# Kernel tuning notes

Hardware: AMD Instinct MI355X
Metric: run time of the kernel (lower is better)

## Reference

```python
import jax, jax.numpy as jnp
import numpy as np

B, S, HID = 2, 2048, 4096
H, KVH, D = 32, 8, 128
THETA = 10000.0
SCALE = D ** -0.5


def _rope(x, positions):
    # x: [B, S, nH, D], positions: [B, S] int. Neox style: rotate halves.
    half = D // 2
    inv_freq = 1.0 / (THETA ** (jnp.arange(0, half, dtype=jnp.float32) / half))
    ang = positions.astype(jnp.float32)[..., None] * inv_freq  # [B,S,half]
    cos = jnp.cos(ang)[:, :, None, :]  # [B,S,1,half]
    sin = jnp.sin(ang)[:, :, None, :]
    x1, x2 = x[..., :half], x[..., half:]
    return jnp.concatenate([x1 * cos - x2 * sin, x2 * cos + x1 * sin], axis=-1)


def setup_inputs() -> dict:
    key = jax.random.key(0)
    k1, k2, k3, k4, k5 = jax.random.split(key, 5)
    std_in = HID ** -0.5
    return {
        "positions": jnp.tile(jnp.arange(S, dtype=jnp.int32), (B, 1)),
        "hidden_states": jax.random.normal(k1, (B, S, HID), jnp.float32),
        "wq": jax.random.normal(k2, (HID, H * D), jnp.float32) * std_in,
        "wk": jax.random.normal(k3, (HID, KVH * D), jnp.float32) * std_in,
        "wv": jax.random.normal(k4, (HID, KVH * D), jnp.float32) * std_in,
        "wo": jax.random.normal(k5, (H * D, HID), jnp.float32) * ((H * D) ** -0.5),
    }


def reference(positions, hidden_states, wq, wk, wv, wo):
    # Separate Q/K/V projections (bias=False)
    q = (hidden_states @ wq).reshape(B, S, H, D)
    k = (hidden_states @ wk).reshape(B, S, KVH, D)
    v = (hidden_states @ wv).reshape(B, S, KVH, D)
    # RoPE on q and k
    q = _rope(q, positions)
    k = _rope(k, positions)
    # GQA: expand KV heads to query heads
    group = H // KVH
    k = jnp.repeat(k, group, axis=2)  # [B,S,H,D]
    v = jnp.repeat(v, group, axis=2)
    # Causal scaled dot-product attention
    scores = jnp.einsum("bqhd,bkhd->bhqk", q, k) * SCALE
    causal = jnp.tril(jnp.ones((S, S), dtype=bool))
    scores = jnp.where(causal, scores, jnp.finfo(scores.dtype).min)
    probs = jax.nn.softmax(scores, axis=-1)
    attn = jnp.einsum("bhqk,bkhd->bqhd", probs, v).reshape(B, S, H * D)
    return attn @ wo
```

## Files before the change

kernel.cpp:

```cpp
#include <hip/hip_runtime.h>
#include <cstdint>

typedef __bf16 bf16;
typedef __attribute__((ext_vector_type(4))) __bf16 bf16x4;
typedef __attribute__((ext_vector_type(8))) __bf16 bf16x8;
typedef __attribute__((ext_vector_type(4))) float f32x4;

#define DEVI __device__ __forceinline__

#define BATCH 2
#define SEQ 2048
#define HID 4096
#define NH 32
#define NKVH 8
#define HD 128
#define QKVN 6144
#define MROWS 4096
#define ATT_SCALE 0.08838834764831845f
#define QSCALE (0.08838834764831845f * 1.4426950408889634f)
#define ROPE_C (-0.2076205059304601f)

DEVI void gload_lds16(const bf16* g, bf16* l) {
  __builtin_amdgcn_global_load_lds(
      (__attribute__((address_space(1))) void*)(g),
      (__attribute__((address_space(3))) void*)(l), 16, 0, 0);
}

__global__ void h2b_kernel(const float* __restrict__ in, bf16* __restrict__ out) {
  long i = ((long)blockIdx.x * 256 + threadIdx.x) * 4;
  float4 v = *(const float4*)(in + i);
  bf16x4 o;
  o[0] = (bf16)v.x; o[1] = (bf16)v.y; o[2] = (bf16)v.z; o[3] = (bf16)v.w;
  *(bf16x4*)(out + i) = o;
}

__global__ void wtrans_kernel(const float* __restrict__ in, bf16* __restrict__ out,
                              int K, int N) {
  __shared__ float t[64][65];
  int n0 = blockIdx.x * 64, k0 = blockIdx.y * 64;
  int tid = threadIdx.x;
  int tx = tid & 15, ty = tid >> 4;
#pragma unroll
  for (int rr = 0; rr < 4; ++rr) {
    int k = ty * 4 + rr;
    float4 v = *(const float4*)(in + (long)(k0 + k) * N + n0 + tx * 4);
    t[k][tx * 4 + 0] = v.x; t[k][tx * 4 + 1] = v.y;
    t[k][tx * 4 + 2] = v.z; t[k][tx * 4 + 3] = v.w;
  }
  __syncthreads();
  int kc = tid & 7, nn = tid >> 3;
#pragma unroll
  for (int pp = 0; pp < 2; ++pp) {
    int n = nn + pp * 32;
    bf16x8 o;
#pragma unroll
    for (int j = 0; j < 8; ++j) o[j] = (bf16)t[kc * 8 + j][n];
    *(bf16x8*)(out + (long)(n0 + n) * K + k0 + kc * 8) = o;
  }
}

__global__ void ropek_kernel(bf16* __restrict__ qkv, const int* __restrict__ pos) {
  long t = (long)blockIdx.x * 256 + threadIdx.x;
  int d8 = (int)(t & 7) * 8;
  long u = t >> 3;
  int hh = (int)(u % 8);
  int row = (int)(u / 8);
  float p = (float)pos[row];
  bf16* base = qkv + (long)row * QKVN + 4096 + hh * HD + d8;
  bf16x8 x1v = *(const bf16x8*)(base);
  bf16x8 x2v = *(const bf16x8*)(base + 64);
  bf16x8 o1, o2;
#pragma unroll
  for (int j = 0; j < 8; ++j) {
    float ang = p * exp2f((float)(d8 + j) * ROPE_C);
    float sn, cs;
    __sincosf(ang, &sn, &cs);
    float x1 = (float)x1v[j], x2 = (float)x2v[j];
    o1[j] = (bf16)(x1 * cs - x2 * sn);
    o2[j] = (bf16)(x2 * cs + x1 * sn);
  }
  *(bf16x8*)(base) = o1;
  *(bf16x8*)(base + 64) = o2;
}

__global__ void vtrans_kernel(const bf16* __restrict__ qkv, bf16* __restrict__ vt) {
  __shared__ bf16 t[32][33];
  int s0 = blockIdx.x * 32, d0 = blockIdx.y * 32, bk = blockIdx.z;
  int b = bk >> 3, kvh = bk & 7;
  int tx = threadIdx.x, ty = threadIdx.y;
#pragma unroll
  for (int r = 0; r < 4; ++r) {
    int s = ty + r * 8;
    t[s][tx] = qkv[(long)(b * SEQ + s0 + s) * QKVN + 5120 + kvh * HD + d0 + tx];
  }
  __syncthreads();
#pragma unroll
  for (int r = 0; r < 4; ++r) {
    int d = ty + r * 8;
    vt[((long)bk * HD + d0 + d) * SEQ + s0 + tx] = t[tx][d];
  }
}

template <typename OutT>
__global__ __launch_bounds__(512, 2)
void gemm256(const bf16* __restrict__ A, const bf16* __restrict__ BT,
             OutT* __restrict__ C, int M, int N, int K) {
  extern __shared__ __align__(16) bf16 lds[];
  const int tid = threadIdx.x;
  const int lane = tid & 63, wave = tid >> 6;
  const int wm = wave >> 1, wn = wave & 1;
  const int l16 = lane & 15, lhi = lane >> 4;
  const int nwg = gridDim.x * gridDim.y;
  const int bid = blockIdx.y * gridDim.x + blockIdx.x;
  const int cpx = nwg >> 3;
  const int swz = (bid & 7) * cpx + (bid >> 3);
  const int bx = swz % gridDim.x, by = swz / gridDim.x;
  const long bm0 = (long)by * 256, bn0 = (long)bx * 128;

  const int srow8 = lane >> 3;
  const int scol = (lane & 7) ^ srow8;

  const int NT = K >> 6;
  f32x4 acc[4][4] = {};

  auto stage = [&](int slot, int t) {
    const long k0 = (long)t << 6;
    bf16* dst = lds + slot * 24576;
#pragma unroll
    for (int i = 0; i < 4; ++i) {
      int r = (wave * 4 + i) * 8 + srow8;
      gload_lds16(A + (bm0 + r) * K + k0 + scol * 8,
                  dst + (wave * 4 + i) * 512 + lane * 8);
    }
#pragma unroll
    for (int i = 0; i < 2; ++i) {
      int r = (wave * 2 + i) * 8 + srow8;
      gload_lds16(BT + (bn0 + r) * K + k0 + scol * 8,
                  dst + 16384 + (wave * 2 + i) * 512 + lane * 8);
    }
  };

  stage(0, 0);
  stage(1, 1);

  for (int t = 0; t < NT; ++t) {
    asm volatile("s_waitcnt vmcnt(6)" ::: "memory");
    __builtin_amdgcn_s_barrier();
    __builtin_amdgcn_sched_barrier(0);
    const int nxt = (t + 2 < NT) ? t + 2 : NT - 1;
    stage((t + 2) % 3, nxt);
    const bf16* As = lds + (t % 3) * 24576;
    const bf16* Bs = As + 16384;
#pragma unroll
    for (int kk = 0; kk < 2; ++kk) {
      bf16x8 af[4], bw[4];
#pragma unroll
      for (int i = 0; i < 4; ++i) {
        int ar = wm * 64 + i * 16 + l16;
        af[i] = *(const bf16x8*)(As + ar * 64 + (((kk * 4 + lhi) ^ (ar & 7))) * 8);
        int br = wn * 64 + i * 16 + l16;
        bw[i] = *(const bf16x8*)(Bs + br * 64 + (((kk * 4 + lhi) ^ (br & 7))) * 8);
      }
      __builtin_amdgcn_s_setprio(1);
#pragma unroll
      for (int i = 0; i < 4; ++i)
#pragma unroll
        for (int j = 0; j < 4; ++j)
          acc[i][j] = __builtin_amdgcn_mfma_f32_16x16x32_bf16(af[i], bw[j], acc[i][j], 0, 0, 0);
      __builtin_amdgcn_s_setprio(0);
    }
  }
  asm volatile("s_waitcnt vmcnt(0)" ::: "memory");
#pragma unroll
  for (int i = 0; i < 4; ++i)
#pragma unroll
    for (int r = 0; r < 4; ++r) {
      long grow = bm0 + wm * 64 + i * 16 + lhi * 4 + r;
#pragma unroll
      for (int j = 0; j < 4; ++j) {
        long gcol = bn0 + wn * 64 + j * 16 + l16;
        C[grow * N + gcol] = (OutT)acc[i][j][r];
      }
    }
}

template <typename OutT>
__global__ __launch_bounds__(512, 2)
void gemm8p(const bf16* __restrict__ A, const bf16* __restrict__ BT,
            OutT* __restrict__ C, int M, int N, int K) {
  extern __shared__ __align__(16) bf16 lds[];
  const int tid = threadIdx.x;
  const int lane = tid & 63, wave = tid >> 6;
  const int wm = wave >> 2, wn = wave & 3;
  const int l16 = lane & 15, lhi = lane >> 4;
  const int nwg = gridDim.x * gridDim.y;
  const int bid = blockIdx.y * gridDim.x + blockIdx.x;
  const int cpx = nwg >> 3;
  const int swz = (bid & 7) * cpx + (bid >> 3);
  const int bx = swz % gridDim.x, by = swz / gridDim.x;
  const long bm0 = (long)by * 256, bn0 = (long)bx * 256;

  bf16* Alds = lds;
  bf16* Blds = lds + 32768;
  const int NT = K >> 6;

  f32x4 acc[8][4] = {};

  auto stageH = [&](const bf16* src, long row0, long k0, bf16* dst) {
#pragma unroll
    for (int j = 0; j < 2; ++j) {
      int r = j * 64 + (tid >> 3);
      int sc = (tid & 7) ^ (r & 7);
      gload_lds16(src + (row0 + r) * (long)K + k0 + sc * 8,
                  dst + j * 4096 + tid * 8);
    }
  };

  stageH(A, bm0, 0, Alds);
  stageH(A, bm0 + 128, 0, Alds + 8192);
  stageH(BT, bn0, 0, Blds);
  stageH(BT, bn0 + 128, 0, Blds + 8192);
  {
    long k1p = (NT > 1) ? 64 : 0;
    stageH(A, bm0, k1p, Alds + 16384);
    stageH(BT, bn0, k1p, Blds + 16384);
    stageH(BT, bn0 + 128, k1p, Blds + 24576);
  }
  asm volatile("s_waitcnt vmcnt(6)" ::: "memory");
  __builtin_amdgcn_s_barrier();

  const int arow0 = wm * 128 + l16;
  const int brow0 = wn * 64 + l16;

  for (int t = 0; t < NT; ++t) {
    const bf16* Ab = Alds + (t & 1) * 16384;
    const bf16* Bb = Blds + (t & 1) * 16384;
    bf16* Aopp = Alds + ((t + 1) & 1) * 16384;
    bf16* Asame = Alds + (t & 1) * 16384;
    bf16* Bsame = Blds + (t & 1) * 16384;
    const long k1 = (long)((t + 1 < NT) ? t + 1 : NT - 1) << 6;
    const long k2 = (long)((t + 2 < NT) ? t + 2 : NT - 1) << 6;

    bf16x8 a0[4][2], a1[4][2], b0[2][2], b1[2][2];
#pragma unroll
    for (int i = 0; i < 4; ++i) {
      int mr = arow0 + i * 16;
#pragma unroll
      for (int kk = 0; kk < 2; ++kk)
        a0[i][kk] = *(const bf16x8*)(Ab + mr * 64 + (((kk * 4 + lhi) ^ (mr & 7))) * 8);
    }
#pragma unroll
    for (int n = 0; n < 2; ++n) {
      int br = brow0 + n * 16;
#pragma unroll
      for (int kk = 0; kk < 2; ++kk)
        b0[n][kk] = *(const bf16x8*)(Bb + br * 64 + (((kk * 4 + lhi) ^ (br & 7))) * 8);
    }
    __builtin_amdgcn_s_barrier();
    asm volatile("s_waitcnt lgkmcnt(0)" ::: "memory");
    __builtin_amdgcn_sched_barrier(0);
    __builtin_amdgcn_s_setprio(1);
#pragma unroll
    for (int i = 0; i < 4; ++i)
#pragma unroll
      for (int n = 0; n < 2; ++n)
#pragma unroll
        for (int kk = 0; kk < 2; ++kk)
          acc[i][n] = __builtin_amdgcn_mfma_f32_16x16x32_bf16(a0[i][kk], b0[n][kk], acc[i][n], 0, 0, 0);
    __builtin_amdgcn_s_setprio(0);
    __builtin_amdgcn_s_barrier();
#pragma unroll
    for (int i = 0; i < 4; ++i) {
      int mr = arow0 + 64 + i * 16;
#pragma unroll
      for (int kk = 0; kk < 2; ++kk)
        a1[i][kk] = *(const bf16x8*)(Ab + mr * 64 + (((kk * 4 + lhi) ^ (mr & 7))) * 8);
    }
    stageH(A, bm0 + 128, k1, Aopp + 8192);
    __builtin_amdgcn_s_barrier();
    asm volatile("s_waitcnt lgkmcnt(0)" ::: "memory");
    __builtin_amdgcn_sched_barrier(0);
    __builtin_amdgcn_s_setprio(1);
#pragma unroll
    for (int i = 0; i < 4; ++i)
#pragma unroll
      for (int n = 0; n < 2; ++n)
#pragma unroll
        for (int kk = 0; kk < 2; ++kk)
          acc[4 + i][n] = __builtin_amdgcn_mfma_f32_16x16x32_bf16(a1[i][kk], b0[n][kk], acc[4 + i][n], 0, 0, 0);
    __builtin_amdgcn_s_setprio(0);
    __builtin_amdgcn_s_barrier();
#pragma unroll
    for (int n = 0; n < 2; ++n) {
      int br = brow0 + (n + 2) * 16;
#pragma unroll
      for (int kk = 0; kk < 2; ++kk)
        b1[n][kk] = *(const bf16x8*)(Bb + br * 64 + (((kk * 4 + lhi) ^ (br & 7))) * 8);
    }
    stageH(A, bm0, k2, Asame);
    __builtin_amdgcn_s_barrier();
    asm volatile("s_waitcnt lgkmcnt(0)" ::: "memory");
    __builtin_amdgcn_sched_barrier(0);
    __builtin_amdgcn_s_setprio(1);
#pragma unroll
    for (int i = 0; i < 4; ++i)
#pragma unroll
      for (int n = 0; n < 2; ++n)
#pragma unroll
        for (int kk = 0; kk < 2; ++kk)
          acc[4 + i][n + 2] = __builtin_amdgcn_mfma_f32_16x16x32_bf16(a1[i][kk], b1[n][kk], acc[4 + i][n + 2], 0, 0, 0);
    __builtin_amdgcn_s_setprio(0);
    __builtin_amdgcn_s_barrier();
    stageH(BT, bn0, k2, Bsame);
    stageH(BT, bn0 + 128, k2, Bsame + 8192);
    __builtin_amdgcn_s_barrier();
    __builtin_amdgcn_s_setprio(1);
#pragma unroll
    for (int i = 0; i < 4; ++i)
#pragma unroll
      for (int n = 0; n < 2; ++n)
#pragma unroll
        for (int kk = 0; kk < 2; ++kk)
          acc[i][n + 2] = __builtin_amdgcn_mfma_f32_16x16x32_bf16(a0[i][kk], b1[n][kk], acc[i][n + 2], 0, 0, 0);
    __builtin_amdgcn_s_setprio(0);
    asm volatile("s_waitcnt vmcnt(6)" ::: "memory");
    __builtin_amdgcn_s_barrier();
  }
  asm volatile("s_waitcnt vmcnt(0)" ::: "memory");
#pragma unroll
  for (int mi = 0; mi < 8; ++mi)
#pragma unroll
    for (int r = 0; r < 4; ++r) {
      long grow = bm0 + wm * 128 + mi * 16 + lhi * 4 + r;
#pragma unroll
      for (int n = 0; n < 4; ++n) {
        long gcol = bn0 + wn * 64 + n * 16 + l16;
        C[grow * N + gcol] = (OutT)acc[mi][n][r];
      }
    }
}

__global__ __launch_bounds__(512, 4)
void attn_kernel(const bf16* __restrict__ qkv, const bf16* __restrict__ vt,
                 const int* __restrict__ pos, bf16* __restrict__ out) {
  extern __shared__ __align__(16) bf16 smem[];
  const int pi = blockIdx.x, h = blockIdx.y, b = blockIdx.z;
  const int kvh = h >> 2;
  const int tid = threadIdx.x, lane = tid & 63, wave = tid >> 6;
  const int l16 = lane & 15, lhi = lane >> 4;
  const int kloc = lhi * 4;
  bf16* Pw = smem + 32768 + wave * 1024;

  const bf16* kpan = qkv + (long)(b * SEQ) * QKVN + 4096 + kvh * HD;
  const bf16* vpan = vt + (long)(b * NKVH + kvh) * HD * SEQ;

  auto stageKV = [&](int buf, int step) {
    const int kv0 = step * 64;
    bf16* kd = smem + buf * 8192;
    bf16* vd = smem + 16384 + buf * 8192;
#pragma unroll
    for (int i = 0; i < 2; ++i) {
      int kr = wave * 8 + i * 4 + lhi;
      gload_lds16(kpan + (long)(kv0 + kr) * QKVN + (l16 ^ (kr & 7)) * 8,
                  kd + (wave * 8 + i * 4) * 128);
      int vr = wave * 16 + i * 8 + (lane >> 3);
      gload_lds16(vpan + (long)vr * SEQ + kv0 + ((lane & 7) ^ (vr & 7)) * 8,
                  vd + (wave * 16 + i * 8) * 64);
    }
  };

  auto process_chunk = [&](int q0, int nsteps) {
    const int qrow = q0 + wave * 16 + l16;
    float p = (float)pos[b * SEQ + qrow];
    const bf16* qb = qkv + (long)(b * SEQ + qrow) * QKVN + h * HD + lhi * 8;
    bf16x8 raw[4];
#pragma unroll
    for (int di = 0; di < 4; ++di) raw[di] = *(const bf16x8*)(qb + di * 32);
    bf16x8 qf[4];
#pragma unroll
    for (int pr = 0; pr < 2; ++pr)
#pragma unroll
      for (int j = 0; j < 8; ++j) {
        int d = lhi * 8 + pr * 32 + j;
        float ang = p * exp2f((float)d * ROPE_C);
        float sn, cs;
        __sincosf(ang, &sn, &cs);
        float x1 = (float)raw[pr][j], x2 = (float)raw[pr + 2][j];
        qf[pr][j] = (bf16)((x1 * cs - x2 * sn) * QSCALE);
        qf[pr + 2][j] = (bf16)((x2 * cs + x1 * sn) * QSCALE);
      }

    f32x4 oacc[8] = {};
    float m_run = -1e30f, l_run = 0.f;
    const int qg = qrow;
    const int qwmin = q0 + wave * 16;

    stageKV(0, 0);
    asm volatile("s_waitcnt vmcnt(0)" ::: "memory");
    __builtin_amdgcn_s_barrier();

    for (int step = 0; step < nsteps; ++step) {
      const int kv0 = step * 64;
      const int cur = step & 1;
      if (step + 1 < nsteps) {
        stageKV(cur ^ 1, step + 1);
        asm volatile("s_waitcnt vmcnt(4)" ::: "memory");
      } else {
        asm volatile("s_waitcnt vmcnt(0)" ::: "memory");
      }
      const bf16* Kc = smem + cur * 8192;
      const bf16* Vc = smem + 16384 + cur * 8192;

      f32x4 s[4];
      __builtin_amdgcn_s_setprio(1);
#pragma unroll
      for (int c = 0; c < 4; ++c) {
        s[c] = (f32x4){0.f, 0.f, 0.f, 0.f};
        int kr = c * 16 + l16;
#pragma unroll
        for (int di = 0; di < 4; ++di) {
          bf16x8 kf = *(const bf16x8*)(Kc + kr * 128 + (((di * 4 + lhi) ^ (kr & 7))) * 8);
          s[c] = __builtin_amdgcn_mfma_f32_16x16x32_bf16(kf, qf[di], s[c], 0, 0, 0);
        }
      }
      __builtin_amdgcn_s_setprio(0);
      if (kv0 + 63 > qwmin) {
#pragma unroll
        for (int c = 0; c < 4; ++c)
#pragma unroll
          for (int r = 0; r < 4; ++r) {
            int kcol = kv0 + c * 16 + kloc + r;
            if (kcol > qg) s[c][r] = -1e30f;
          }
      }
      float mloc = s[0][0];
#pragma unroll
      for (int c = 0; c < 4; ++c)
#pragma unroll
        for (int r = 0; r < 4; ++r) mloc = fmaxf(mloc, s[c][r]);
      mloc = fmaxf(mloc, __shfl_xor(mloc, 16, 64));
      mloc = fmaxf(mloc, __shfl_xor(mloc, 32, 64));
      bool skip = __all(mloc - m_run <= 8.0f);
      float alpha = 1.f;
      if (!skip) {
        float mn = fmaxf(m_run, mloc);
        alpha = exp2f(m_run - mn);
        m_run = mn;
      }
      float sm = 0.f;
      bf16x4 pb[4];
#pragma unroll
      for (int c = 0; c < 4; ++c)
#pragma unroll
        for (int r = 0; r < 4; ++r) {
          float pv = exp2f(s[c][r] - m_run);
          sm += pv;
          pb[c][r] = (bf16)pv;
        }
      sm += __shfl_xor(sm, 16, 64);
      sm += __shfl_xor(sm, 32, 64);
      l_run = l_run * alpha + sm;
#pragma unroll
      for (int c = 0; c < 4; ++c) {
        int sl = (c * 2 + (lhi >> 1)) ^ (l16 & 7);
        *(bf16x4*)(Pw + l16 * 64 + sl * 8 + (lhi & 1) * 4) = pb[c];
      }
      if (!skip) {
        float a_o[4];
#pragma unroll
        for (int r = 0; r < 4; ++r) a_o[r] = __shfl(alpha, kloc + r, 64);
#pragma unroll
        for (int dj = 0; dj < 8; ++dj)
#pragma unroll
          for (int r = 0; r < 4; ++r) oacc[dj][r] *= a_o[r];
      }
      __builtin_amdgcn_s_setprio(1);
#pragma unroll
      for (int kh = 0; kh < 2; ++kh) {
        bf16x8 pf = *(const bf16x8*)(Pw + l16 * 64 + (((kh * 4 + lhi) ^ (l16 & 7))) * 8);
#pragma unroll
        for (int dj = 0; dj < 8; ++dj) {
          int vr = dj * 16 + l16;
          bf16x8 vf = *(const bf16x8*)(Vc + vr * 64 + (((kh * 4 + lhi) ^ (vr & 7))) * 8);
          oacc[dj] = __builtin_amdgcn_mfma_f32_16x16x32_bf16(pf, vf, oacc[dj], 0, 0, 0);
        }
      }
      __builtin_amdgcn_s_setprio(0);
      __builtin_amdgcn_s_barrier();
    }
    float linv[4];
#pragma unroll
    for (int r = 0; r < 4; ++r) linv[r] = 1.f / __shfl(l_run, kloc + r, 64);
#pragma unroll
    for (int r = 0; r < 4; ++r) {
      long orow = (long)(b * SEQ + q0 + wave * 16 + lhi * 4 + r);
#pragma unroll
      for (int dj = 0; dj < 8; ++dj)
        out[orow * (NH * HD) + h * HD + dj * 16 + l16] = (bf16)(oacc[dj][r] * linv[r]);
    }
  };

  process_chunk(pi * 128, 2 * pi + 2);
  process_chunk((15 - pi) * 128, 32 - 2 * pi);
}

extern "C" void kernel_launch(void* const* d_in, const int* in_sizes, int n_in,
                              void* d_out, int out_size, void* d_ws, size_t ws_size,
                              hipStream_t stream) {
  const int* positions = (const int*)d_in[0];
  const float* hidden = (const float*)d_in[1];
  const float* wq = (const float*)d_in[2];
  const float* wk = (const float*)d_in[3];
  const float* wv = (const float*)d_in[4];
  const float* wo = (const float*)d_in[5];
  float* out = (float*)d_out;
  char* ws = (char*)d_ws;

  const size_t SZ_H = (size_t)MROWS * HID * 2;
  const size_t SZ_WQKV = (size_t)QKVN * HID * 2;
  const size_t SZ_WO = (size_t)HID * HID * 2;
  bf16* h_bf = (bf16*)(ws);
  bf16* wqkvT = (bf16*)(ws + SZ_H);
  bf16* woT = (bf16*)(ws + SZ_H + SZ_WQKV);
  bf16* qkv = (bf16*)(ws + SZ_H + SZ_WQKV + SZ_WO);
  bf16* attn = h_bf;
  bf16* vtbuf = wqkvT;

  const int G8P_SMEM = 131072;
  const int R3_SMEM = 3 * 24576 * 2;
  const int ATTN_SMEM = 40960 * 2;
  auto* g1 = gemm256<bf16>;
  auto* g2 = gemm8p<float>;
  hipFuncSetAttribute(reinterpret_cast<const void*>(g1),
                      hipFuncAttributeMaxDynamicSharedMemorySize, R3_SMEM);
  hipFuncSetAttribute(reinterpret_cast<const void*>(g2),
                      hipFuncAttributeMaxDynamicSharedMemorySize, G8P_SMEM);
  hipFuncSetAttribute(reinterpret_cast<const void*>(attn_kernel),
                      hipFuncAttributeMaxDynamicSharedMemorySize, ATTN_SMEM);

  h2b_kernel<<<(MROWS * (long)HID) / (256 * 4), 256, 0, stream>>>(hidden, h_bf);
  wtrans_kernel<<<dim3(HID / 64, HID / 64), 256, 0, stream>>>(wq, wqkvT, HID, HID);
  wtrans_kernel<<<dim3(1024 / 64, HID / 64), 256, 0, stream>>>(wk, wqkvT + (long)4096 * HID, HID, 1024);
  wtrans_kernel<<<dim3(1024 / 64, HID / 64), 256, 0, stream>>>(wv, wqkvT + (long)5120 * HID, HID, 1024);
  wtrans_kernel<<<dim3(HID / 64, HID / 64), 256, 0, stream>>>(wo, woT, HID, HID);
  gemm256<bf16><<<dim3(QKVN / 128, MROWS / 256), 512, R3_SMEM, stream>>>(h_bf, wqkvT, qkv, MROWS, QKVN, HID);
  ropek_kernel<<<(MROWS * 8 * 8) / 256, 256, 0, stream>>>(qkv, positions);
  dim3 t32(32, 8);
  vtrans_kernel<<<dim3(SEQ / 32, HD / 32, BATCH * NKVH), t32, 0, stream>>>(qkv, vtbuf);
  attn_kernel<<<dim3(8, NH, BATCH), 512, ATTN_SMEM, stream>>>(qkv, vtbuf, positions, attn);
  gemm8p<float><<<dim3(HID / 256, MROWS / 256), 512, G8P_SMEM, stream>>>(attn, woT, out, MROWS, HID, HID);
}
```

Baseline: 509.7 us.

## Process two 16-row query tiles per wave in attention to reuse K/V fragments

Each wave in the attention kernel now handles 32 query rows as two 16-row tiles (A and B). Both tiles share each K and V fragment read from LDS, so a block covers 256 query rows and the grid is halved. The goal is to halve LDS reads and K/V staging per unit of work. In exchange, register pressure doubles, which leads to lowering the launch-bounds occupancy hint from 4 to 2, and there are fewer blocks to spread across the GPU.

```diff
diff --git a/kernel.cpp b/kernel.cpp
--- a/kernel.cpp
+++ b/kernel.cpp
@@ -340,7 +340,7 @@
     }
 }
 
-__global__ __launch_bounds__(512, 4)
+__global__ __launch_bounds__(512, 2)
 void attn_kernel(const bf16* __restrict__ qkv, const bf16* __restrict__ vt,
                  const int* __restrict__ pos, bf16* __restrict__ out) {
   extern __shared__ __align__(16) bf16 smem[];
@@ -349,7 +349,8 @@
   const int tid = threadIdx.x, lane = tid & 63, wave = tid >> 6;
   const int l16 = lane & 15, lhi = lane >> 4;
   const int kloc = lhi * 4;
-  bf16* Pw = smem + 32768 + wave * 1024;
+  bf16* PwA = smem + 32768 + wave * 2048;
+  bf16* PwB = PwA + 1024;
 
   const bf16* kpan = qkv + (long)(b * SEQ) * QKVN + 4096 + kvh * HD;
   const bf16* vpan = vt + (long)(b * NKVH + kvh) * HD * SEQ;
@@ -370,30 +371,42 @@
   };
 
   auto process_chunk = [&](int q0, int nsteps) {
-    const int qrow = q0 + wave * 16 + l16;
-    float p = (float)pos[b * SEQ + qrow];
-    const bf16* qb = qkv + (long)(b * SEQ + qrow) * QKVN + h * HD + lhi * 8;
-    bf16x8 raw[4];
-#pragma unroll
-    for (int di = 0; di < 4; ++di) raw[di] = *(const bf16x8*)(qb + di * 32);
-    bf16x8 qf[4];
-#pragma unroll
-    for (int pr = 0; pr < 2; ++pr)
-#pragma unroll
-      for (int j = 0; j < 8; ++j) {
-        int d = lhi * 8 + pr * 32 + j;
-        float ang = p * exp2f((float)d * ROPE_C);
-        float sn, cs;
-        __sincosf(ang, &sn, &cs);
-        float x1 = (float)raw[pr][j], x2 = (float)raw[pr + 2][j];
-        qf[pr][j] = (bf16)((x1 * cs - x2 * sn) * QSCALE);
-        qf[pr + 2][j] = (bf16)((x2 * cs + x1 * sn) * QSCALE);
-      }
-
-    f32x4 oacc[8] = {};
-    float m_run = -1e30f, l_run = 0.f;
-    const int qg = qrow;
-    const int qwmin = q0 + wave * 16;
+    const int qrowA = q0 + wave * 32 + l16;
+    const int qrowB = qrowA + 16;
+    bf16x8 qfA[4], qfB[4];
+    {
+      float pA = (float)pos[b * SEQ + qrowA];
+      float pB = (float)pos[b * SEQ + qrowB];
+      const bf16* qbA = qkv + (long)(b * SEQ + qrowA) * QKVN + h * HD + lhi * 8;
+      const bf16* qbB = qkv + (long)(b * SEQ + qrowB) * QKVN + h * HD + lhi * 8;
+      bf16x8 rawA[4], rawB[4];
+#pragma unroll
+      for (int di = 0; di < 4; ++di) {
+        rawA[di] = *(const bf16x8*)(qbA + di * 32);
+        rawB[di] = *(const bf16x8*)(qbB + di * 32);
+      }
+#pragma unroll
+      for (int pr = 0; pr < 2; ++pr)
+#pragma unroll
+        for (int j = 0; j < 8; ++j) {
+          int d = lhi * 8 + pr * 32 + j;
+          float f = exp2f((float)d * ROPE_C);
+          float snA, csA, snB, csB;
+          __sincosf(pA * f, &snA, &csA);
+          __sincosf(pB * f, &snB, &csB);
+          float x1 = (float)rawA[pr][j], x2 = (float)rawA[pr + 2][j];
+          qfA[pr][j] = (bf16)((x1 * csA - x2 * snA) * QSCALE);
+          qfA[pr + 2][j] = (bf16)((x2 * csA + x1 * snA) * QSCALE);
+          float y1 = (float)rawB[pr][j], y2 = (float)rawB[pr + 2][j];
+          qfB[pr][j] = (bf16)((y1 * csB - y2 * snB) * QSCALE);
+          qfB[pr + 2][j] = (bf16)((y2 * csB + y1 * snB) * QSCALE);
+        }
+    }
+
+    f32x4 oaccA[8] = {}, oaccB[8] = {};
+    float m_runA = -1e30f, l_runA = 0.f, m_runB = -1e30f, l_runB = 0.f;
+    const int qwminA = q0 + wave * 32;
+    const int qwminB = qwminA + 16;
 
     stageKV(0, 0);
     asm volatile("s_waitcnt vmcnt(0)" ::: "memory");
@@ -411,97 +424,161 @@
       const bf16* Kc = smem + cur * 8192;
       const bf16* Vc = smem + 16384 + cur * 8192;
 
-      f32x4 s[4];
+      f32x4 sA[4], sB[4];
       __builtin_amdgcn_s_setprio(1);
 #pragma unroll
       for (int c = 0; c < 4; ++c) {
-        s[c] = (f32x4){0.f, 0.f, 0.f, 0.f};
+        sA[c] = (f32x4){0.f, 0.f, 0.f, 0.f};
+        sB[c] = (f32x4){0.f, 0.f, 0.f, 0.f};
         int kr = c * 16 + l16;
 #pragma unroll
         for (int di = 0; di < 4; ++di) {
           bf16x8 kf = *(const bf16x8*)(Kc + kr * 128 + (((di * 4 + lhi) ^ (kr & 7))) * 8);
-          s[c] = __builtin_amdgcn_mfma_f32_16x16x32_bf16(kf, qf[di], s[c], 0, 0, 0);
+          sA[c] = __builtin_amdgcn_mfma_f32_16x16x32_bf16(kf, qfA[di], sA[c], 0, 0, 0);
+          sB[c] = __builtin_amdgcn_mfma_f32_16x16x32_bf16(kf, qfB[di], sB[c], 0, 0, 0);
         }
       }
       __builtin_amdgcn_s_setprio(0);
-      if (kv0 + 63 > qwmin) {
+      if (kv0 + 63 > qwminA) {
 #pragma unroll
         for (int c = 0; c < 4; ++c)
 #pragma unroll
           for (int r = 0; r < 4; ++r) {
             int kcol = kv0 + c * 16 + kloc + r;
-            if (kcol > qg) s[c][r] = -1e30f;
+            if (kcol > qrowA) sA[c][r] = -1e30f;
           }
       }
-      float mloc = s[0][0];
-#pragma unroll
-      for (int c = 0; c < 4; ++c)
-#pragma unroll
-        for (int r = 0; r < 4; ++r) mloc = fmaxf(mloc, s[c][r]);
-      mloc = fmaxf(mloc, __shfl_xor(mloc, 16, 64));
-      mloc = fmaxf(mloc, __shfl_xor(mloc, 32, 64));
-      bool skip = __all(mloc - m_run <= 8.0f);
-      float alpha = 1.f;
-      if (!skip) {
-        float mn = fmaxf(m_run, mloc);
-        alpha = exp2f(m_run - mn);
-        m_run = mn;
-      }
-      float sm = 0.f;
-      bf16x4 pb[4];
-#pragma unroll
-      for (int c = 0; c < 4; ++c)
-#pragma unroll
-        for (int r = 0; r < 4; ++r) {
-          float pv = exp2f(s[c][r] - m_run);
-          sm += pv;
-          pb[c][r] = (bf16)pv;
-        }
-      sm += __shfl_xor(sm, 16, 64);
-      sm += __shfl_xor(sm, 32, 64);
-      l_run = l_run * alpha + sm;
-#pragma unroll
-      for (int c = 0; c < 4; ++c) {
-        int sl = (c * 2 + (lhi >> 1)) ^ (l16 & 7);
-        *(bf16x4*)(Pw + l16 * 64 + sl * 8 + (lhi & 1) * 4) = pb[c];
-      }
-      if (!skip) {
-        float a_o[4];
-#pragma unroll
-        for (int r = 0; r < 4; ++r) a_o[r] = __shfl(alpha, kloc + r, 64);
-#pragma unroll
-        for (int dj = 0; dj < 8; ++dj)
-#pragma unroll
-          for (int r = 0; r < 4; ++r) oacc[dj][r] *= a_o[r];
+      if (kv0 + 63 > qwminB) {
+#pragma unroll
+        for (int c = 0; c < 4; ++c)
+#pragma unroll
+          for (int r = 0; r < 4; ++r) {
+            int kcol = kv0 + c * 16 + kloc + r;
+            if (kcol > qrowB) sB[c][r] = -1e30f;
+          }
+      }
+      {
+        float mloc = sA[0][0];
+#pragma unroll
+        for (int c = 0; c < 4; ++c)
+#pragma unroll
+          for (int r = 0; r < 4; ++r) mloc = fmaxf(mloc, sA[c][r]);
+        mloc = fmaxf(mloc, __shfl_xor(mloc, 16, 64));
+        mloc = fmaxf(mloc, __shfl_xor(mloc, 32, 64));
+        bool skip = __all(mloc - m_runA <= 8.0f);
+        float alpha = 1.f;
+        if (!skip) {
+          float mn = fmaxf(m_runA, mloc);
+          alpha = exp2f(m_runA - mn);
+          m_runA = mn;
+        }
+        float sm = 0.f;
+        bf16x4 pb[4];
+#pragma unroll
+        for (int c = 0; c < 4; ++c)
+#pragma unroll
+          for (int r = 0; r < 4; ++r) {
+            float pv = exp2f(sA[c][r] - m_runA);
+            sm += pv;
+            pb[c][r] = (bf16)pv;
+          }
+        sm += __shfl_xor(sm, 16, 64);
+        sm += __shfl_xor(sm, 32, 64);
+        l_runA = l_runA * alpha + sm;
+#pragma unroll
+        for (int c = 0; c < 4; ++c) {
+          int sl = (c * 2 + (lhi >> 1)) ^ (l16 & 7);
+          *(bf16x4*)(PwA + l16 * 64 + sl * 8 + (lhi & 1) * 4) = pb[c];
+        }
+        if (!skip) {
+          float a_o[4];
+#pragma unroll
+          for (int r = 0; r < 4; ++r) a_o[r] = __shfl(alpha, kloc + r, 64);
+#pragma unroll
+          for (int dj = 0; dj < 8; ++dj)
+#pragma unroll
+            for (int r = 0; r < 4; ++r) oaccA[dj][r] *= a_o[r];
+        }
+      }
+      {
+        float mloc = sB[0][0];
+#pragma unroll
+        for (int c = 0; c < 4; ++c)
+#pragma unroll
+          for (int r = 0; r < 4; ++r) mloc = fmaxf(mloc, sB[c][r]);
+        mloc = fmaxf(mloc, __shfl_xor(mloc, 16, 64));
+        mloc = fmaxf(mloc, __shfl_xor(mloc, 32, 64));
+        bool skip = __all(mloc - m_runB <= 8.0f);
+        float alpha = 1.f;
+        if (!skip) {
+          float mn = fmaxf(m_runB, mloc);
+          alpha = exp2f(m_runB - mn);
+          m_runB = mn;
+        }
+        float sm = 0.f;
+        bf16x4 pb[4];
+#pragma unroll
+        for (int c = 0; c < 4; ++c)
+#pragma unroll
+          for (int r = 0; r < 4; ++r) {
+            float pv = exp2f(sB[c][r] - m_runB);
+            sm += pv;
+            pb[c][r] = (bf16)pv;
+          }
+        sm += __shfl_xor(sm, 16, 64);
+        sm += __shfl_xor(sm, 32, 64);
+        l_runB = l_runB * alpha + sm;
+#pragma unroll
+        for (int c = 0; c < 4; ++c) {
+          int sl = (c * 2 + (lhi >> 1)) ^ (l16 & 7);
+          *(bf16x4*)(PwB + l16 * 64 + sl * 8 + (lhi & 1) * 4) = pb[c];
+        }
+        if (!skip) {
+          float a_o[4];
+#pragma unroll
+          for (int r = 0; r < 4; ++r) a_o[r] = __shfl(alpha, kloc + r, 64);
+#pragma unroll
+          for (int dj = 0; dj < 8; ++dj)
+#pragma unroll
+            for (int r = 0; r < 4; ++r) oaccB[dj][r] *= a_o[r];
+        }
       }
       __builtin_amdgcn_s_setprio(1);
 #pragma unroll
       for (int kh = 0; kh < 2; ++kh) {
-        bf16x8 pf = *(const bf16x8*)(Pw + l16 * 64 + (((kh * 4 + lhi) ^ (l16 & 7))) * 8);
+        bf16x8 pfA = *(const bf16x8*)(PwA + l16 * 64 + (((kh * 4 + lhi) ^ (l16 & 7))) * 8);
+        bf16x8 pfB = *(const bf16x8*)(PwB + l16 * 64 + (((kh * 4 + lhi) ^ (l16 & 7))) * 8);
 #pragma unroll
         for (int dj = 0; dj < 8; ++dj) {
           int vr = dj * 16 + l16;
           bf16x8 vf = *(const bf16x8*)(Vc + vr * 64 + (((kh * 4 + lhi) ^ (vr & 7))) * 8);
-          oacc[dj] = __builtin_amdgcn_mfma_f32_16x16x32_bf16(pf, vf, oacc[dj], 0, 0, 0);
+          oaccA[dj] = __builtin_amdgcn_mfma_f32_16x16x32_bf16(pfA, vf, oaccA[dj], 0, 0, 0);
+          oaccB[dj] = __builtin_amdgcn_mfma_f32_16x16x32_bf16(pfB, vf, oaccB[dj], 0, 0, 0);
         }
       }
       __builtin_amdgcn_s_setprio(0);
       __builtin_amdgcn_s_barrier();
     }
-    float linv[4];
-#pragma unroll
-    for (int r = 0; r < 4; ++r) linv[r] = 1.f / __shfl(l_run, kloc + r, 64);
+    float linvA[4], linvB[4];
 #pragma unroll
     for (int r = 0; r < 4; ++r) {
-      long orow = (long)(b * SEQ + q0 + wave * 16 + lhi * 4 + r);
-#pragma unroll
-      for (int dj = 0; dj < 8; ++dj)
-        out[orow * (NH * HD) + h * HD + dj * 16 + l16] = (bf16)(oacc[dj][r] * linv[r]);
+      linvA[r] = 1.f / __shfl(l_runA, kloc + r, 64);
+      linvB[r] = 1.f / __shfl(l_runB, kloc + r, 64);
+    }
+#pragma unroll
+    for (int r = 0; r < 4; ++r) {
+      long orowA = (long)(b * SEQ + q0 + wave * 32 + lhi * 4 + r);
+      long orowB = orowA + 16;
+#pragma unroll
+      for (int dj = 0; dj < 8; ++dj) {
+        out[orowA * (NH * HD) + h * HD + dj * 16 + l16] = (bf16)(oaccA[dj][r] * linvA[r]);
+        out[orowB * (NH * HD) + h * HD + dj * 16 + l16] = (bf16)(oaccB[dj][r] * linvB[r]);
+      }
     }
   };
 
-  process_chunk(pi * 128, 2 * pi + 2);
-  process_chunk((15 - pi) * 128, 32 - 2 * pi);
+  process_chunk(pi * 256, 4 * pi + 4);
+  process_chunk((7 - pi) * 256, 32 - 4 * pi);
 }
 
 extern "C" void kernel_launch(void* const* d_in, const int* in_sizes, int n_in,
@@ -528,7 +605,7 @@
 
   const int G8P_SMEM = 131072;
   const int R3_SMEM = 3 * 24576 * 2;
-  const int ATTN_SMEM = 40960 * 2;
+  const int ATTN_SMEM = 98304;
   auto* g1 = gemm256<bf16>;
   auto* g2 = gemm8p<float>;
   hipFuncSetAttribute(reinterpret_cast<const void*>(g1),
@@ -547,6 +624,6 @@
   ropek_kernel<<<(MROWS * 8 * 8) / 256, 256, 0, stream>>>(qkv, positions);
   dim3 t32(32, 8);
   vtrans_kernel<<<dim3(SEQ / 32, HD / 32, BATCH * NKVH), t32, 0, stream>>>(qkv, vtbuf);
-  attn_kernel<<<dim3(8, NH, BATCH), 512, ATTN_SMEM, stream>>>(qkv, vtbuf, positions, attn);
+  attn_kernel<<<dim3(4, NH, BATCH), 512, ATTN_SMEM, stream>>>(qkv, vtbuf, positions, attn);
   gemm8p<float><<<dim3(HID / 256, MROWS / 256), 512, G8P_SMEM, stream>>>(attn, woT, out, MROWS, HID, HID);
 }
```

New measurement: 521.0 us. +2.2%, slower.
